# Kernel tuning notes

Measured on AMD Instinct MI355X. Metric: run time of the kernel, lower is better.

Reference implementation:

```python
import jax, jax.numpy as jnp
import numpy as np

N_MLP = 16
LATENT = 1024
S0, S1, S2, OUT = 512, 256, 128, 3


def _make_grid(n_grid_step):
    # matches np.meshgrid (indexing='xy') then reshape(-1): points (x, y)
    p = np.linspace(-1.0, 1.0, n_grid_step, dtype=np.float32)
    X, Y = np.meshgrid(p, p)
    return jnp.asarray(np.stack([X.ravel(), Y.ravel()], axis=-1))  # [G, 2]


def setup_inputs() -> dict:
    key = jax.random.key(0)
    ks = jax.random.split(key, 12)
    sc = lambda fan_in: 1.0 / np.sqrt(fan_in)
    inp = {
        "x0": jax.random.normal(ks[0], (LATENT,), jnp.float32),
        "W0a": jax.random.normal(ks[1], (N_MLP, S0, LATENT), jnp.float32) * sc(LATENT),
        "b0a": jax.random.normal(ks[2], (N_MLP, S0), jnp.float32) * sc(LATENT),
        "W0b": jax.random.normal(ks[3], (N_MLP, S0, 2), jnp.float32) * sc(2),
        "b0b": jax.random.normal(ks[4], (N_MLP, S0), jnp.float32) * sc(2),
        "W1": jax.random.normal(ks[5], (N_MLP, S1, S0), jnp.float32) * sc(S0),
        "b1": jax.random.normal(ks[6], (N_MLP, S1), jnp.float32) * sc(S0),
        "W2": jax.random.normal(ks[7], (N_MLP, S2, S1), jnp.float32) * sc(S1),
        "b2": jax.random.normal(ks[8], (N_MLP, S2), jnp.float32) * sc(S1),
        "W3": jax.random.normal(ks[9], (N_MLP, OUT, S2), jnp.float32) * sc(S2),
        "b3": jax.random.normal(ks[10], (N_MLP, OUT), jnp.float32) * sc(S2),
        "n_grid_step": 128,
    }
    return inp


def reference(x0, W0a, b0a, W0b, b0b, W1, b1, W2, b2, W3, b3, n_grid_step):
    grid = _make_grid(n_grid_step)  # [G, 2], constant (requires_grad=False)
    # latent branch: [m, S0]
    y0_a = jnp.einsum('mol,l->mo', W0a, x0) + b0a
    # grid branch: [m, G, S0]
    y0_b = jnp.einsum('moi,gi->mgo', W0b, grid) + b0b[:, None, :]
    h = jax.nn.relu(y0_a[:, None, :] + y0_b)                        # [m,G,S0]
    h = jax.nn.relu(jnp.einsum('moh,mgh->mgo', W1, h) + b1[:, None, :])  # [m,G,S1]
    h = jax.nn.relu(jnp.einsum('moh,mgh->mgo', W2, h) + b2[:, None, :])  # [m,G,S2]
    out = jnp.tanh(jnp.einsum('moh,mgh->mgo', W3, h) + b3[:, None, :])   # [m,G,3]
    return out.reshape(-1, OUT)  # [m*G, 3]
```

## Files before the change

kernel.cpp:

```cpp
#include <hip/hip_runtime.h>
#include <hip/hip_bf16.h>
#include <cstdint>

typedef __bf16 bf16_t;
typedef bf16_t bf16x8 __attribute__((ext_vector_type(8)));
typedef bf16_t bf16x4 __attribute__((ext_vector_type(4)));
typedef float  f32x4  __attribute__((ext_vector_type(4)));

#define S0 512
#define S1 256
#define S2 128
#define NGRID 128
#define GPTS (NGRID*NGRID)

#define WS_BASE  0u
#define WS_W1P   32768u
#define WS_W2P   4227072u
#define WS_W3P   5275648u
#define WS_BASEC 5341184u
#define WS_WXYC  5373952u
#define WS_IDX   5439488u
#define WS_LIN   5472256u
#define WS_F     5505024u
#define WS_CNT   5570560u

__device__ __forceinline__ float tanh_fast(float x) {
  float e = __builtin_amdgcn_exp2f(x * 2.88539008f);
  return fmaf(-2.0f, __builtin_amdgcn_rcpf(e + 1.0f), 1.0f);
}

__global__ __launch_bounds__(256) void prep_a(
    const float* __restrict__ x0, const float* __restrict__ W0a,
    const float* __restrict__ b0a, const float* __restrict__ b0b,
    const float* __restrict__ W2, const float* __restrict__ W3,
    float* __restrict__ base, bf16_t* __restrict__ W2p, bf16_t* __restrict__ W3p)
{
  if (blockIdx.x < 2048) {
    int wid = (blockIdx.x << 2) + (threadIdx.x >> 6);
    int L = threadIdx.x & 63;
    int m = wid >> 9, o = wid & 511;
    const float* wrow = W0a + ((size_t)(m*S0 + o) << 10);
    float acc = 0.f;
#pragma unroll
    for (int i = 0; i < 4; ++i) {
      f32x4 wv = *(const f32x4*)(wrow + i*256 + L*4);
      f32x4 xv = *(const f32x4*)(x0   + i*256 + L*4);
      acc += wv.x*xv.x + wv.y*xv.y + wv.z*xv.z + wv.w*xv.w;
    }
#pragma unroll
    for (int s = 32; s; s >>= 1) acc += __shfl_xor(acc, s, 64);
    if (L == 0) base[m*S0 + o] = acc + b0a[m*S0 + o] + b0b[m*S0 + o];
    return;
  }

  int T = (blockIdx.x - 2048) * 256 + threadIdx.x;
  const float* src = nullptr;
  bf16_t* dst = nullptr;
  if (T < 65536) {
    int L = T & 63, nt = (T >> 6) & 7, ks = (T >> 9) & 7, m = T >> 12;
    int n = nt*16 + (L & 15), k0 = ks*32 + ((L >> 4) & 3)*8;
    src = W2 + (size_t)(m*S2 + n)*S1 + k0;
    dst = W2p + (size_t)T*8;
  } else {
    int T3 = T - 65536;
    int L = T3 & 63, ks = (T3 >> 6) & 3, m = T3 >> 8;
    int n = L & 15, k0 = ks*32 + ((L >> 4) & 3)*8;
    dst = W3p + (size_t)T3*8;
    if (n < 3) src = W3 + (size_t)(m*3 + n)*S2 + k0;
  }
  bf16x8 v;
  if (src) {
    f32x4 a = *(const f32x4*)src;
    f32x4 b = *(const f32x4*)(src + 4);
    v[0]=(bf16_t)a.x; v[1]=(bf16_t)a.y; v[2]=(bf16_t)a.z; v[3]=(bf16_t)a.w;
    v[4]=(bf16_t)b.x; v[5]=(bf16_t)b.y; v[6]=(bf16_t)b.z; v[7]=(bf16_t)b.w;
  } else {
#pragma unroll
    for (int j = 0; j < 8; ++j) v[j] = (bf16_t)0.f;
  }
  *(bf16x8*)dst = v;
}

__global__ __launch_bounds__(256) void classify_k(
    const float* __restrict__ base, const float* __restrict__ W0b,
    float* __restrict__ basec, float* __restrict__ wxyc,
    int* __restrict__ idx, int* __restrict__ lin,
    int* __restrict__ Kc, int* __restrict__ nlin, float* __restrict__ F)
{
  __shared__ int sc[512];
  const int m = blockIdx.x, t = threadIdx.x;
  float b[2], wx[2], wy[2]; int fa[2], fl[2];
#pragma unroll
  for (int h = 0; h < 2; ++h) {
    const int k = t + h*256;
    b[h]  = base[m*S0 + k];
    wx[h] = W0b[(m*S0 + k)*2];
    wy[h] = W0b[(m*S0 + k)*2 + 1];
    const float aw = fabsf(wx[h]) + fabsf(wy[h]);
    const int dead = (b[h] + aw) <= 0.f;
    fl[h] = (!dead) && ((b[h] - aw) >= 0.f);
    fa[h] = (!dead) && (!fl[h]);
    sc[k] = fa[h] | (fl[h] << 16);
  }
  __syncthreads();
  for (int off = 1; off < 512; off <<= 1) {
    int v0 = sc[t], v1 = sc[t+256];
    int u0 = (t >= off) ? sc[t-off] : 0;
    int u1 = (t+256 >= off) ? sc[t+256-off] : 0;
    __syncthreads();
    sc[t] = v0 + u0; sc[t+256] = v1 + u1;
    __syncthreads();
  }
  const int tot = sc[511];
  const int KcM = tot & 0xffff, nlM = tot >> 16;
#pragma unroll
  for (int h = 0; h < 2; ++h) {
    const int k = t + h*256;
    const int incl = sc[k];
    if (fa[h]) {
      const int p = (incl & 0xffff) - 1;
      idx[m*S0 + p] = k;
      basec[m*S0 + p] = b[h];
      wxyc[m*S0*2 + 2*p]     = wx[h];
      wxyc[m*S0*2 + 2*p + 1] = wy[h];
    } else if (fl[h]) {
      lin[m*S0 + ((incl >> 16) - 1)] = k;
    }
  }
  for (int s = t; s < 512; s += 256) {
    if (s >= KcM) {
      idx[m*S0 + s] = 0;
      basec[m*S0 + s] = 0.f;
      wxyc[m*S0*2 + 2*s] = 0.f;
      wxyc[m*S0*2 + 2*s + 1] = 0.f;
    }
  }
  for (int i = t; i < 1024; i += 256) F[m*1024 + i] = 0.f;
  if (t == 0) { Kc[m] = KcM; nlin[m] = nlM; }
}

__global__ __launch_bounds__(256) void prep_b(
    const float* __restrict__ W1, const float* __restrict__ base,
    const float* __restrict__ W0b,
    const int* __restrict__ idx, const int* __restrict__ lin,
    const int* __restrict__ Kc, const int* __restrict__ nlin,
    bf16_t* __restrict__ W1p, float* __restrict__ F)
{
  if (blockIdx.x < 1024) {
    const int T = blockIdx.x*256 + threadIdx.x;
    const int L = T & 63, nt = (T >> 6) & 15, ks = (T >> 10) & 15, m = T >> 14;
    const int KcM = Kc[m];
    const int n = nt*16 + (L & 15), kb = ks*32 + ((L >> 4) & 3)*8;
    const float* wrow = W1 + (size_t)(m*S1 + n)*S0;
    const int* ip = idx + m*S0 + kb;
    bf16x8 v;
#pragma unroll
    for (int j = 0; j < 8; ++j)
      v[j] = (kb + j < KcM) ? (bf16_t)wrow[ip[j]] : (bf16_t)0.f;
    *(bf16x8*)(W1p + (size_t)T*8) = v;
  } else {
    const int b2 = blockIdx.x - 1024;
    const int m = b2 >> 4, s = b2 & 15, n = threadIdx.x;
    const int nl = nlin[m];
    float a0 = 0.f, ax = 0.f, ay = 0.f;
    const float* wrow = W1 + (size_t)(m*S1 + n)*S0;
    for (int j = s; j < nl; j += 16) {
      const int k = lin[m*S0 + j];
      const float w = wrow[k];
      a0 = fmaf(w, base[m*S0 + k], a0);
      ax = fmaf(w, W0b[(m*S0 + k)*2], ax);
      ay = fmaf(w, W0b[(m*S0 + k)*2 + 1], ay);
    }
    float* fp = F + ((size_t)m*S1 + n)*4;
    atomicAdd(fp + 0, a0);
    atomicAdd(fp + 1, ax);
    atomicAdd(fp + 2, ay);
  }
}

template<int NKS>
__device__ __forceinline__ void l1_compute(
    const bf16_t* __restrict__ bp1, const float* __restrict__ bc,
    const float* __restrict__ wc, bf16_t* sStg,
    const int w, const int L, const int quad, const float yv,
    const float xrw, f32x4 (&acc1)[4][4])
{
  bf16x8 Bc[4];
#pragma unroll
  for (int n = 0; n < 4; ++n) Bc[n] = *(const bf16x8*)(bp1 + (size_t)n*512);

#pragma unroll 2
  for (int ks = 0; ks < NKS; ++ks) {
    const int kk = ks*32 + quad*8;

    bf16x8 Bn[4];
    if (ks + 1 < NKS) {
#pragma unroll
      for (int n = 0; n < 4; ++n)
        Bn[n] = *(const bf16x8*)(bp1 + (size_t)(ks+1)*8192 + (size_t)n*512);
    }

    f32x4 cA  = *(const f32x4*)(bc + kk);
    f32x4 cB  = *(const f32x4*)(bc + kk + 4);
    f32x4 wv0 = *(const f32x4*)(wc + kk*2);
    f32x4 wv1 = *(const f32x4*)(wc + kk*2 + 4);
    f32x4 wv2 = *(const f32x4*)(wc + kk*2 + 8);
    f32x4 wv3 = *(const f32x4*)(wc + kk*2 + 12);
    bf16x8 g;
    g[0] = (bf16_t)fmaxf(fmaf(wv0.x, xrw, fmaf(wv0.y, yv, cA.x)), 0.f);
    g[1] = (bf16_t)fmaxf(fmaf(wv0.z, xrw, fmaf(wv0.w, yv, cA.y)), 0.f);
    g[2] = (bf16_t)fmaxf(fmaf(wv1.x, xrw, fmaf(wv1.y, yv, cA.z)), 0.f);
    g[3] = (bf16_t)fmaxf(fmaf(wv1.z, xrw, fmaf(wv1.w, yv, cA.w)), 0.f);
    g[4] = (bf16_t)fmaxf(fmaf(wv2.x, xrw, fmaf(wv2.y, yv, cB.x)), 0.f);
    g[5] = (bf16_t)fmaxf(fmaf(wv2.z, xrw, fmaf(wv2.w, yv, cB.y)), 0.f);
    g[6] = (bf16_t)fmaxf(fmaf(wv3.x, xrw, fmaf(wv3.y, yv, cB.z)), 0.f);
    g[7] = (bf16_t)fmaxf(fmaf(wv3.z, xrw, fmaf(wv3.w, yv, cB.w)), 0.f);

    bf16_t* stg = sStg + (ks & 1)*2048;
    *(bf16x8*)(stg + ((w << 6) + L)*8) = g;
    asm volatile("s_waitcnt lgkmcnt(0)" ::: "memory");
    __builtin_amdgcn_s_barrier();
    __builtin_amdgcn_sched_barrier(0);

#pragma unroll
    for (int mt = 0; mt < 4; ++mt) {
      bf16x8 af;
      if (mt == w) af = g;
      else         af = *(const bf16x8*)(stg + ((mt << 6) + L)*8);
#pragma unroll
      for (int n = 0; n < 4; ++n)
        acc1[mt][n] = __builtin_amdgcn_mfma_f32_16x16x32_bf16(Bc[n], af, acc1[mt][n], 0, 0, 0);
    }
    if (ks + 1 < NKS) {
#pragma unroll
      for (int n = 0; n < 4; ++n) Bc[n] = Bn[n];
    }
  }
}

__global__ __launch_bounds__(256, 3) void fused_mlp_k(
    const float* __restrict__ basec, const float* __restrict__ wxyc,
    const float* __restrict__ F, const int* __restrict__ Kc,
    const bf16_t* __restrict__ W1p, const bf16_t* __restrict__ W2p,
    const bf16_t* __restrict__ W3p,
    const float* __restrict__ b1, const float* __restrict__ b2,
    const float* __restrict__ b3, float* __restrict__ out)
{
  __shared__ __align__(16) bf16_t sA1[64*264];

  const int bid  = blockIdx.x;
  const int m    = bid >> 8;
  const int tile = bid & 255;
  const int g0   = tile * 64;

  const int tid  = threadIdx.x;
  const int w    = tid >> 6, L = tid & 63;
  const int quad = L >> 4, lrow = L & 15;

  const float step = 2.0f / 127.0f;
  const float yv  = -1.0f + (float)(tile >> 1) * step;
  const float xv0 = -1.0f + (float)(((tile & 1) << 6) + lrow) * step;
  const float xrw = xv0 + (float)(w*16)*step;

  const float* bc = basec + m*S0;
  const float* wc = wxyc + m*(S0*2);
  const int nks = (Kc[m] + 31) >> 5;

  f32x4 zero = {0.f, 0.f, 0.f, 0.f};
  f32x4 acc1[4][4];
#pragma unroll
  for (int a = 0; a < 4; ++a)
#pragma unroll
    for (int b = 0; b < 4; ++b) acc1[a][b] = zero;

  const bf16_t* bp1 = W1p + (((size_t)(m*16)*16 + w*4)*64 + L)*8;
#define L1_CASE(NN) case NN: l1_compute<NN>(bp1, bc, wc, sA1, w, L, quad, yv, xrw, acc1); break;
  switch (nks) {
    L1_CASE(16) L1_CASE(15) L1_CASE(14) L1_CASE(13)
    L1_CASE(12) L1_CASE(11) L1_CASE(10) L1_CASE(9)
    L1_CASE(8)  L1_CASE(7)  L1_CASE(6)  L1_CASE(5)
    L1_CASE(4)  L1_CASE(3)  L1_CASE(2)  L1_CASE(1)
    default: break;
  }
#undef L1_CASE
  __syncthreads();

#pragma unroll
  for (int nb = 0; nb < 4; ++nb) {
    const int col = w*64 + nb*16 + quad*4;
    f32x4 bb = *(const f32x4*)(b1 + m*S1 + col);
    float cterm[4], fx[4];
#pragma unroll
    for (int p = 0; p < 4; ++p) {
      f32x4 Fv = *(const f32x4*)(F + ((size_t)m*S1 + col + p)*4);
      cterm[p] = fmaf(Fv.z, yv, bb[p] + Fv.x);
      fx[p] = Fv.y;
    }
#pragma unroll
    for (int mt = 0; mt < 4; ++mt) {
      const int row = mt*16 + lrow;
      const float xr = xv0 + (float)(mt*16)*step;
      bf16x4 v;
#pragma unroll
      for (int p = 0; p < 4; ++p)
        v[p] = (bf16_t)fmaxf(acc1[mt][nb][p] + fmaf(fx[p], xr, cterm[p]), 0.f);
      *(bf16x4*)(&sA1[row*264 + col]) = v;
    }
  }
  __syncthreads();

  f32x4 acc2[4][2];
#pragma unroll
  for (int a = 0; a < 4; ++a) { acc2[a][0] = zero; acc2[a][1] = zero; }
  const bf16_t* bp2 = W2p + (((size_t)(m*8)*8 + w*2)*64 + L)*8;
#pragma unroll 2
  for (int ks = 0; ks < 8; ++ks) {
    const int k2 = ks*32 + quad*8;
    bf16x8 af[4];
#pragma unroll
    for (int mt = 0; mt < 4; ++mt)
      af[mt] = *(const bf16x8*)(&sA1[(mt*16 + lrow)*264 + k2]);
    bf16x8 b0f = *(const bf16x8*)(bp2 + (size_t)ks*4096);
    bf16x8 b1f = *(const bf16x8*)(bp2 + (size_t)ks*4096 + 512);
#pragma unroll
    for (int mt = 0; mt < 4; ++mt)
      acc2[mt][0] = __builtin_amdgcn_mfma_f32_16x16x32_bf16(b0f, af[mt], acc2[mt][0], 0, 0, 0);
#pragma unroll
    for (int mt = 0; mt < 4; ++mt)
      acc2[mt][1] = __builtin_amdgcn_mfma_f32_16x16x32_bf16(b1f, af[mt], acc2[mt][1], 0, 0, 0);
  }
  __syncthreads();

  bf16_t* sH2 = sA1;
#pragma unroll
  for (int nb = 0; nb < 2; ++nb) {
    const int col = w*32 + nb*16 + quad*4;
    f32x4 bb = *(const f32x4*)(b2 + m*S2 + col);
#pragma unroll
    for (int mt = 0; mt < 4; ++mt) {
      const int row = mt*16 + lrow;
      bf16x4 v;
#pragma unroll
      for (int p = 0; p < 4; ++p)
        v[p] = (bf16_t)fmaxf(acc2[mt][nb][p] + bb[p], 0.f);
      *(bf16x4*)(&sH2[row*136 + col]) = v;
    }
  }
  __syncthreads();

  f32x4 acc3 = zero;
#pragma unroll
  for (int ks = 0; ks < 4; ++ks) {
    bf16x8 af  = *(const bf16x8*)(&sH2[(w*16 + lrow)*136 + ks*32 + quad*8]);
    bf16x8 bfr = *(const bf16x8*)(W3p + (((size_t)m*4 + ks)*64 + L)*8);
    acc3 = __builtin_amdgcn_mfma_f32_16x16x32_bf16(bfr, af, acc3, 0, 0, 0);
  }
  if (quad == 0) {
    const size_t o = ((size_t)m*GPTS + g0 + w*16 + lrow)*3;
    out[o + 0] = tanh_fast(acc3[0] + b3[m*3 + 0]);
    out[o + 1] = tanh_fast(acc3[1] + b3[m*3 + 1]);
    out[o + 2] = tanh_fast(acc3[2] + b3[m*3 + 2]);
  }
}

extern "C" void kernel_launch(void* const* d_in, const int* in_sizes, int n_in,
                              void* d_out, int out_size, void* d_ws, size_t ws_size,
                              hipStream_t stream) {
  const float* x0  = (const float*)d_in[0];
  const float* W0a = (const float*)d_in[1];
  const float* b0a = (const float*)d_in[2];
  const float* W0b = (const float*)d_in[3];
  const float* b0b = (const float*)d_in[4];
  const float* W1  = (const float*)d_in[5];
  const float* b1  = (const float*)d_in[6];
  const float* W2  = (const float*)d_in[7];
  const float* b2  = (const float*)d_in[8];
  const float* W3  = (const float*)d_in[9];
  const float* b3  = (const float*)d_in[10];

  char* ws = (char*)d_ws;
  float*  base  = (float*)(ws + WS_BASE);
  bf16_t* W1p   = (bf16_t*)(ws + WS_W1P);
  bf16_t* W2p   = (bf16_t*)(ws + WS_W2P);
  bf16_t* W3p   = (bf16_t*)(ws + WS_W3P);
  float*  basec = (float*)(ws + WS_BASEC);
  float*  wxyc  = (float*)(ws + WS_WXYC);
  int*    idx   = (int*)(ws + WS_IDX);
  int*    lin   = (int*)(ws + WS_LIN);
  float*  F     = (float*)(ws + WS_F);
  int*    Kc    = (int*)(ws + WS_CNT);
  int*    nlin  = (int*)(ws + WS_CNT + 64);
  float*  out   = (float*)d_out;

  prep_a<<<2368, 256, 0, stream>>>(x0, W0a, b0a, b0b, W2, W3, base, W2p, W3p);
  classify_k<<<16, 256, 0, stream>>>(base, W0b, basec, wxyc, idx, lin, Kc, nlin, F);
  prep_b<<<1280, 256, 0, stream>>>(W1, base, W0b, idx, lin, Kc, nlin, W1p, F);
  fused_mlp_k<<<4096, 256, 0, stream>>>(basec, wxyc, F, Kc, W1p, W2p, W3p, b1, b2, b3, out);
}
```

Baseline: 207.6 us.

## Split fused MLP tile across 8 waves with 2x4 warp grid

```diff
diff --git a/kernel.cpp b/kernel.cpp
--- a/kernel.cpp
+++ b/kernel.cpp
@@ -182,63 +182,62 @@
 __device__ __forceinline__ void l1_compute(
     const bf16_t* __restrict__ bp1, const float* __restrict__ bc,
     const float* __restrict__ wc, bf16_t* sStg,
-    const int w, const int L, const int quad, const float yv,
-    const float xrw, f32x4 (&acc1)[4][4])
-{
-  bf16x8 Bc[4];
-#pragma unroll
-  for (int n = 0; n < 4; ++n) Bc[n] = *(const bf16x8*)(bp1 + (size_t)n*512);
+    const int w, const int L, const int quad, const int wrh,
+    const float yv, const float xrw, f32x4 (&acc1)[2][4])
+{
+  bf16x8 B0[2], B1[2];
+  B0[0] = *(const bf16x8*)(bp1);
+  B0[1] = *(const bf16x8*)(bp1 + 512);
 
 #pragma unroll 2
   for (int ks = 0; ks < NKS; ++ks) {
+    const bf16_t* bpk = bp1 + (size_t)ks*8192;
+    B1[0] = *(const bf16x8*)(bpk + 1024);
+    B1[1] = *(const bf16x8*)(bpk + 1536);
+
     const int kk = ks*32 + quad*8;
-
-    bf16x8 Bn[4];
-    if (ks + 1 < NKS) {
-#pragma unroll
-      for (int n = 0; n < 4; ++n)
-        Bn[n] = *(const bf16x8*)(bp1 + (size_t)(ks+1)*8192 + (size_t)n*512);
-    }
-
-    f32x4 cA  = *(const f32x4*)(bc + kk);
-    f32x4 cB  = *(const f32x4*)(bc + kk + 4);
-    f32x4 wv0 = *(const f32x4*)(wc + kk*2);
-    f32x4 wv1 = *(const f32x4*)(wc + kk*2 + 4);
-    f32x4 wv2 = *(const f32x4*)(wc + kk*2 + 8);
-    f32x4 wv3 = *(const f32x4*)(wc + kk*2 + 12);
-    bf16x8 g;
-    g[0] = (bf16_t)fmaxf(fmaf(wv0.x, xrw, fmaf(wv0.y, yv, cA.x)), 0.f);
-    g[1] = (bf16_t)fmaxf(fmaf(wv0.z, xrw, fmaf(wv0.w, yv, cA.y)), 0.f);
-    g[2] = (bf16_t)fmaxf(fmaf(wv1.x, xrw, fmaf(wv1.y, yv, cA.z)), 0.f);
-    g[3] = (bf16_t)fmaxf(fmaf(wv1.z, xrw, fmaf(wv1.w, yv, cA.w)), 0.f);
-    g[4] = (bf16_t)fmaxf(fmaf(wv2.x, xrw, fmaf(wv2.y, yv, cB.x)), 0.f);
-    g[5] = (bf16_t)fmaxf(fmaf(wv2.z, xrw, fmaf(wv2.w, yv, cB.y)), 0.f);
-    g[6] = (bf16_t)fmaxf(fmaf(wv3.x, xrw, fmaf(wv3.y, yv, cB.z)), 0.f);
-    g[7] = (bf16_t)fmaxf(fmaf(wv3.z, xrw, fmaf(wv3.w, yv, cB.w)), 0.f);
-
     bf16_t* stg = sStg + (ks & 1)*2048;
-    *(bf16x8*)(stg + ((w << 6) + L)*8) = g;
+    if (w < 4) {
+      f32x4 cA  = *(const f32x4*)(bc + kk);
+      f32x4 cB  = *(const f32x4*)(bc + kk + 4);
+      f32x4 wv0 = *(const f32x4*)(wc + kk*2);
+      f32x4 wv1 = *(const f32x4*)(wc + kk*2 + 4);
+      f32x4 wv2 = *(const f32x4*)(wc + kk*2 + 8);
+      f32x4 wv3 = *(const f32x4*)(wc + kk*2 + 12);
+      bf16x8 g;
+      g[0] = (bf16_t)fmaxf(fmaf(wv0.x, xrw, fmaf(wv0.y, yv, cA.x)), 0.f);
+      g[1] = (bf16_t)fmaxf(fmaf(wv0.z, xrw, fmaf(wv0.w, yv, cA.y)), 0.f);
+      g[2] = (bf16_t)fmaxf(fmaf(wv1.x, xrw, fmaf(wv1.y, yv, cA.z)), 0.f);
+      g[3] = (bf16_t)fmaxf(fmaf(wv1.z, xrw, fmaf(wv1.w, yv, cA.w)), 0.f);
+      g[4] = (bf16_t)fmaxf(fmaf(wv2.x, xrw, fmaf(wv2.y, yv, cB.x)), 0.f);
+      g[5] = (bf16_t)fmaxf(fmaf(wv2.z, xrw, fmaf(wv2.w, yv, cB.y)), 0.f);
+      g[6] = (bf16_t)fmaxf(fmaf(wv3.x, xrw, fmaf(wv3.y, yv, cB.z)), 0.f);
+      g[7] = (bf16_t)fmaxf(fmaf(wv3.z, xrw, fmaf(wv3.w, yv, cB.w)), 0.f);
+      *(bf16x8*)(stg + ((w << 6) + L)*8) = g;
+    }
     asm volatile("s_waitcnt lgkmcnt(0)" ::: "memory");
     __builtin_amdgcn_s_barrier();
     __builtin_amdgcn_sched_barrier(0);
 
-#pragma unroll
-    for (int mt = 0; mt < 4; ++mt) {
-      bf16x8 af;
-      if (mt == w) af = g;
-      else         af = *(const bf16x8*)(stg + ((mt << 6) + L)*8);
-#pragma unroll
-      for (int n = 0; n < 4; ++n)
-        acc1[mt][n] = __builtin_amdgcn_mfma_f32_16x16x32_bf16(Bc[n], af, acc1[mt][n], 0, 0, 0);
-    }
+    bf16x8 af0 = *(const bf16x8*)(stg + (((2*wrh)   << 6) + L)*8);
+    bf16x8 af1 = *(const bf16x8*)(stg + (((2*wrh+1) << 6) + L)*8);
+
+    acc1[0][0] = __builtin_amdgcn_mfma_f32_16x16x32_bf16(B0[0], af0, acc1[0][0], 0, 0, 0);
+    acc1[1][0] = __builtin_amdgcn_mfma_f32_16x16x32_bf16(B0[0], af1, acc1[1][0], 0, 0, 0);
+    acc1[0][1] = __builtin_amdgcn_mfma_f32_16x16x32_bf16(B0[1], af0, acc1[0][1], 0, 0, 0);
+    acc1[1][1] = __builtin_amdgcn_mfma_f32_16x16x32_bf16(B0[1], af1, acc1[1][1], 0, 0, 0);
     if (ks + 1 < NKS) {
-#pragma unroll
-      for (int n = 0; n < 4; ++n) Bc[n] = Bn[n];
-    }
-  }
-}
-
-__global__ __launch_bounds__(256, 3) void fused_mlp_k(
+      B0[0] = *(const bf16x8*)(bpk + 8192);
+      B0[1] = *(const bf16x8*)(bpk + 8192 + 512);
+    }
+    acc1[0][2] = __builtin_amdgcn_mfma_f32_16x16x32_bf16(B1[0], af0, acc1[0][2], 0, 0, 0);
+    acc1[1][2] = __builtin_amdgcn_mfma_f32_16x16x32_bf16(B1[0], af1, acc1[1][2], 0, 0, 0);
+    acc1[0][3] = __builtin_amdgcn_mfma_f32_16x16x32_bf16(B1[1], af0, acc1[0][3], 0, 0, 0);
+    acc1[1][3] = __builtin_amdgcn_mfma_f32_16x16x32_bf16(B1[1], af1, acc1[1][3], 0, 0, 0);
+  }
+}
+
+__global__ __launch_bounds__(512, 4) void fused_mlp_k(
     const float* __restrict__ basec, const float* __restrict__ wxyc,
     const float* __restrict__ F, const int* __restrict__ Kc,
     const bf16_t* __restrict__ W1p, const bf16_t* __restrict__ W2p,
@@ -256,6 +255,8 @@
   const int tid  = threadIdx.x;
   const int w    = tid >> 6, L = tid & 63;
   const int quad = L >> 4, lrow = L & 15;
+  const int wrh  = w >> 2;
+  const int wcq  = w & 3;
 
   const float step = 2.0f / 127.0f;
   const float yv  = -1.0f + (float)(tile >> 1) * step;
@@ -267,14 +268,14 @@
   const int nks = (Kc[m] + 31) >> 5;
 
   f32x4 zero = {0.f, 0.f, 0.f, 0.f};
-  f32x4 acc1[4][4];
-#pragma unroll
-  for (int a = 0; a < 4; ++a)
+  f32x4 acc1[2][4];
+#pragma unroll
+  for (int a = 0; a < 2; ++a)
 #pragma unroll
     for (int b = 0; b < 4; ++b) acc1[a][b] = zero;
 
-  const bf16_t* bp1 = W1p + (((size_t)(m*16)*16 + w*4)*64 + L)*8;
-#define L1_CASE(NN) case NN: l1_compute<NN>(bp1, bc, wc, sA1, w, L, quad, yv, xrw, acc1); break;
+  const bf16_t* bp1 = W1p + (((size_t)(m*16)*16 + wcq*4)*64 + L)*8;
+#define L1_CASE(NN) case NN: l1_compute<NN>(bp1, bc, wc, sA1, w, L, quad, wrh, yv, xrw, acc1); break;
   switch (nks) {
     L1_CASE(16) L1_CASE(15) L1_CASE(14) L1_CASE(13)
     L1_CASE(12) L1_CASE(11) L1_CASE(10) L1_CASE(9)
@@ -287,7 +288,7 @@
 
 #pragma unroll
   for (int nb = 0; nb < 4; ++nb) {
-    const int col = w*64 + nb*16 + quad*4;
+    const int col = wcq*64 + nb*16 + quad*4;
     f32x4 bb = *(const f32x4*)(b1 + m*S1 + col);
     float cterm[4], fx[4];
 #pragma unroll
@@ -297,69 +298,67 @@
       fx[p] = Fv.y;
     }
 #pragma unroll
-    for (int mt = 0; mt < 4; ++mt) {
+    for (int mt2 = 0; mt2 < 2; ++mt2) {
+      const int mt  = 2*wrh + mt2;
       const int row = mt*16 + lrow;
       const float xr = xv0 + (float)(mt*16)*step;
       bf16x4 v;
 #pragma unroll
       for (int p = 0; p < 4; ++p)
-        v[p] = (bf16_t)fmaxf(acc1[mt][nb][p] + fmaf(fx[p], xr, cterm[p]), 0.f);
+        v[p] = (bf16_t)fmaxf(acc1[mt2][nb][p] + fmaf(fx[p], xr, cterm[p]), 0.f);
       *(bf16x4*)(&sA1[row*264 + col]) = v;
     }
   }
   __syncthreads();
 
-  f32x4 acc2[4][2];
-#pragma unroll
-  for (int a = 0; a < 4; ++a) { acc2[a][0] = zero; acc2[a][1] = zero; }
-  const bf16_t* bp2 = W2p + (((size_t)(m*8)*8 + w*2)*64 + L)*8;
+  f32x4 acc2[2][2];
+  acc2[0][0] = zero; acc2[0][1] = zero; acc2[1][0] = zero; acc2[1][1] = zero;
+  const bf16_t* bp2 = W2p + (((size_t)(m*8)*8 + wcq*2)*64 + L)*8;
 #pragma unroll 2
   for (int ks = 0; ks < 8; ++ks) {
     const int k2 = ks*32 + quad*8;
-    bf16x8 af[4];
-#pragma unroll
-    for (int mt = 0; mt < 4; ++mt)
-      af[mt] = *(const bf16x8*)(&sA1[(mt*16 + lrow)*264 + k2]);
+    bf16x8 af0 = *(const bf16x8*)(&sA1[((2*wrh  )*16 + lrow)*264 + k2]);
+    bf16x8 af1 = *(const bf16x8*)(&sA1[((2*wrh+1)*16 + lrow)*264 + k2]);
     bf16x8 b0f = *(const bf16x8*)(bp2 + (size_t)ks*4096);
     bf16x8 b1f = *(const bf16x8*)(bp2 + (size_t)ks*4096 + 512);
-#pragma unroll
-    for (int mt = 0; mt < 4; ++mt)
-      acc2[mt][0] = __builtin_amdgcn_mfma_f32_16x16x32_bf16(b0f, af[mt], acc2[mt][0], 0, 0, 0);
-#pragma unroll
-    for (int mt = 0; mt < 4; ++mt)
-      acc2[mt][1] = __builtin_amdgcn_mfma_f32_16x16x32_bf16(b1f, af[mt], acc2[mt][1], 0, 0, 0);
+    acc2[0][0] = __builtin_amdgcn_mfma_f32_16x16x32_bf16(b0f, af0, acc2[0][0], 0, 0, 0);
+    acc2[1][0] = __builtin_amdgcn_mfma_f32_16x16x32_bf16(b0f, af1, acc2[1][0], 0, 0, 0);
+    acc2[0][1] = __builtin_amdgcn_mfma_f32_16x16x32_bf16(b1f, af0, acc2[0][1], 0, 0, 0);
+    acc2[1][1] = __builtin_amdgcn_mfma_f32_16x16x32_bf16(b1f, af1, acc2[1][1], 0, 0, 0);
   }
   __syncthreads();
 
   bf16_t* sH2 = sA1;
 #pragma unroll
   for (int nb = 0; nb < 2; ++nb) {
-    const int col = w*32 + nb*16 + quad*4;
+    const int col = wcq*32 + nb*16 + quad*4;
     f32x4 bb = *(const f32x4*)(b2 + m*S2 + col);
 #pragma unroll
-    for (int mt = 0; mt < 4; ++mt) {
-      const int row = mt*16 + lrow;
+    for (int mt2 = 0; mt2 < 2; ++mt2) {
+      const int row = (2*wrh + mt2)*16 + lrow;
       bf16x4 v;
 #pragma unroll
       for (int p = 0; p < 4; ++p)
-        v[p] = (bf16_t)fmaxf(acc2[mt][nb][p] + bb[p], 0.f);
+        v[p] = (bf16_t)fmaxf(acc2[mt2][nb][p] + bb[p], 0.f);
       *(bf16x4*)(&sH2[row*136 + col]) = v;
     }
   }
   __syncthreads();
 
-  f32x4 acc3 = zero;
-#pragma unroll
-  for (int ks = 0; ks < 4; ++ks) {
-    bf16x8 af  = *(const bf16x8*)(&sH2[(w*16 + lrow)*136 + ks*32 + quad*8]);
-    bf16x8 bfr = *(const bf16x8*)(W3p + (((size_t)m*4 + ks)*64 + L)*8);
-    acc3 = __builtin_amdgcn_mfma_f32_16x16x32_bf16(bfr, af, acc3, 0, 0, 0);
-  }
-  if (quad == 0) {
-    const size_t o = ((size_t)m*GPTS + g0 + w*16 + lrow)*3;
-    out[o + 0] = tanh_fast(acc3[0] + b3[m*3 + 0]);
-    out[o + 1] = tanh_fast(acc3[1] + b3[m*3 + 1]);
-    out[o + 2] = tanh_fast(acc3[2] + b3[m*3 + 2]);
+  if (w < 4) {
+    f32x4 acc3 = zero;
+#pragma unroll
+    for (int ks = 0; ks < 4; ++ks) {
+      bf16x8 af  = *(const bf16x8*)(&sH2[(w*16 + lrow)*136 + ks*32 + quad*8]);
+      bf16x8 bfr = *(const bf16x8*)(W3p + (((size_t)m*4 + ks)*64 + L)*8);
+      acc3 = __builtin_amdgcn_mfma_f32_16x16x32_bf16(bfr, af, acc3, 0, 0, 0);
+    }
+    if (quad == 0) {
+      const size_t o = ((size_t)m*GPTS + g0 + w*16 + lrow)*3;
+      out[o + 0] = tanh_fast(acc3[0] + b3[m*3 + 0]);
+      out[o + 1] = tanh_fast(acc3[1] + b3[m*3 + 1]);
+      out[o + 2] = tanh_fast(acc3[2] + b3[m*3 + 2]);
+    }
   }
 }
 
@@ -395,5 +394,5 @@
   prep_a<<<2368, 256, 0, stream>>>(x0, W0a, b0a, b0b, W2, W3, base, W2p, W3p);
   classify_k<<<16, 256, 0, stream>>>(base, W0b, basec, wxyc, idx, lin, Kc, nlin, F);
   prep_b<<<1280, 256, 0, stream>>>(W1, base, W0b, idx, lin, Kc, nlin, W1p, F);
-  fused_mlp_k<<<4096, 256, 0, stream>>>(basec, wxyc, F, Kc, W1p, W2p, W3p, b1, b2, b3, out);
-}
+  fused_mlp_k<<<4096, 512, 0, stream>>>(basec, wxyc, F, Kc, W1p, W2p, W3p, b1, b2, b3, out);
+}
```

Measured after the change: 240.3 us. +15.8%, slower.
